# Performance work log

Measured on AMD Instinct MI355X. Metric: run time of the kernel, lower is better.

## Reference

```python
import jax, jax.numpy as jnp
import numpy as np
from jax import lax

STRIDE = 1
PADDING = 1


def setup_inputs() -> dict:
    key = jax.random.key(0)
    k1, k2 = jax.random.split(key)
    x = jax.random.normal(k1, (32, 128, 56, 56), dtype=jnp.float32)
    weight = jax.random.normal(k2, (256, 128, 3, 3), dtype=jnp.float32)
    bias = jnp.zeros((256,), dtype=jnp.float32)
    return {"x": x, "weight": weight, "bias": bias}


def reference(x, weight, bias):
    # Standard 2D cross-correlation (the intended math of the torch
    # unfold + broadcast-multiply + sum implementation):
    #   out[b,o,h,w] = sum_{i,kh,kw} x_pad[b,i,h*s+kh,w*s+kw] * weight[o,i,kh,kw] + bias[o]
    out = lax.conv_general_dilated(
        x, weight,
        window_strides=(STRIDE, STRIDE),
        padding=[(PADDING, PADDING), (PADDING, PADDING)],
        dimension_numbers=("NCHW", "OIHW", "NCHW"),
    )
    return out + bias[None, :, None, None]
```

## Files before the change

### kernel.cpp

```cpp
#include <hip/hip_runtime.h>
#include <cstdint>
#include <cstddef>

#define NB    32
#define CI    128
#define CO    256
#define HW_   56
#define HP    58
#define KTOT  1152
#define NKT   36
#define MTOT  (NB * HW_ * HW_)

static constexpr size_t XP_ELEMS = (size_t)NB * HP * HP * CI;
static constexpr size_t WT_ELEMS = (size_t)CO * KTOT;
static constexpr size_t XP_BYTES = XP_ELEMS * 2;
static constexpr size_t WT_BYTES = WT_ELEMS * 2;

typedef __attribute__((ext_vector_type(8))) short bf16x8;
typedef __attribute__((ext_vector_type(4))) float f32x4;

__device__ __forceinline__ short f32_to_bf16(float f) {
  uint32_t u = __float_as_uint(f);
  uint32_t r = (u + 0x7FFFu + ((u >> 16) & 1u)) >> 16;
  return (short)r;
}

typedef __attribute__((address_space(3))) void       lds_void;
typedef const __attribute__((address_space(1))) void gbl_void;

__device__ __forceinline__ void gload16(const void* g, void* l) {
  __builtin_amdgcn_global_load_lds((gbl_void*)g, (lds_void*)l, 16, 0, 0);
}

__global__ void pad_convert(const float* __restrict__ x, short* __restrict__ xp) {
  __shared__ float lds[CI][57];
  const int blk = blockIdx.x;
  const int hp  = blk % HP;
  const int nb  = blk / HP;
  const int tid = threadIdx.x;
  const bool interior = (hp >= 1 && hp <= HW_);
  if (interior) {
    const float* src = x + (size_t)nb * CI * HW_ * HW_ + (size_t)(hp - 1) * HW_;
    for (int t = tid; t < CI * HW_; t += 256) {
      int c = t / HW_, w = t % HW_;
      lds[c][w] = src[(size_t)c * HW_ * HW_ + w];
    }
  }
  __syncthreads();
  short* dst = xp + (size_t)(nb * HP + hp) * HP * CI;
  for (int t = tid; t < HP * CI; t += 256) {
    int wp = t >> 7, c = t & 127;
    float v = 0.f;
    if (interior && wp >= 1 && wp <= HW_) v = lds[c][wp - 1];
    dst[t] = f32_to_bf16(v);
  }
}

__global__ void wt_convert(const float* __restrict__ wt, short* __restrict__ wbT) {
  int idx = blockIdx.x * 256 + threadIdx.x;
  int c  = idx & 127;
  int t  = idx >> 7;
  int kw = t % 3;  int t2 = t / 3;
  int kh = t2 % 3; int o  = t2 / 3;
  wbT[idx] = f32_to_bf16(wt[(((size_t)o * CI + c) * 3 + kh) * 3 + kw]);
}

__device__ __forceinline__ int tap_off_bytes(int u) {
  const int tap = u >> 2;
  const int cq  = u & 3;
  const int kh  = tap / 3, kw = tap - kh * 3;
  return ((kh * HP + kw) * CI + cq * 32) * 2;
}

__global__ __launch_bounds__(256, 2) void conv_gemm(
    const short* __restrict__ xp, const short* __restrict__ wbT,
    const float* __restrict__ bias, float* __restrict__ out) {
  __shared__ __align__(16) char lds[3 * 24576];

  const int tid = threadIdx.x;
  const int l   = tid & 63;
  const int wv  = tid >> 6;
  const int wm  = wv >> 1, wn = wv & 1;
  const int mt  = blockIdx.x;

  const int piece = l & 3;
  const int srow  = wv * 16 + (l >> 2);
  const char* aP0; const char* aP1;
  {
    int r0 = srow, r1 = 64 + srow;
    int m0 = mt * 128 + r0, m1 = mt * 128 + r1;
    int nb0 = m0 / 3136, hw0 = m0 - nb0 * 3136, h0 = hw0 / HW_, w0 = hw0 - (hw0 / HW_) * HW_;
    int nb1 = m1 / 3136, hw1 = m1 - nb1 * 3136, h1 = hw1 / HW_, w1 = hw1 - (hw1 / HW_) * HW_;
    aP0 = (const char*)xp + ((size_t)((nb0 * HP + h0) * HP + w0) * CI + piece * 8) * 2;
    aP1 = (const char*)xp + ((size_t)((nb1 * HP + h1) * HP + w1) * CI + piece * 8) * 2;
  }
  const char* bP0 = (const char*)wbT + ((size_t)(  0 + srow) * KTOT + piece * 8) * 2;
  const char* bP1 = (const char*)wbT + ((size_t)( 64 + srow) * KTOT + piece * 8) * 2;
  const char* bP2 = (const char*)wbT + ((size_t)(128 + srow) * KTOT + piece * 8) * 2;
  const char* bP3 = (const char*)wbT + ((size_t)(192 + srow) * KTOT + piece * 8) * 2;

  const int raOff = (wm * 64  + (l & 15)) * 64 + (l >> 4) * 16;
  const int rbOff = (wn * 128 + (l & 15)) * 64 + (l >> 4) * 16;

  char* B0 = lds;
  char* B1 = lds + 24576;
  char* B2 = lds + 49152;

#define STAGE(U, BUF)                                                        \
  {                                                                          \
    const int aoff_ = tap_off_bytes(U);                                      \
    const int boff_ = (U) * 64;                                              \
    char* sA_ = (BUF) + wv * 1024;                                           \
    gload16(aP0 + aoff_, sA_);                                               \
    gload16(aP1 + aoff_, sA_ + 4096);                                        \
    char* sB_ = (BUF) + 8192 + wv * 1024;                                    \
    gload16(bP0 + boff_, sB_);                                               \
    gload16(bP1 + boff_, sB_ + 4096);                                        \
    gload16(bP2 + boff_, sB_ + 8192);                                        \
    gload16(bP3 + boff_, sB_ + 12288);                                       \
  }

  f32x4 acc[4][8];
#pragma unroll
  for (int g = 0; g < 4; ++g)
#pragma unroll
    for (int h = 0; h < 8; ++h) acc[g][h] = {0.f, 0.f, 0.f, 0.f};

  STAGE(0, B0)
  STAGE(1, B1)
  asm volatile("s_waitcnt vmcnt(6)" ::: "memory");
  __builtin_amdgcn_s_barrier();
  __builtin_amdgcn_sched_barrier(0);

#define TILE_BODY(V, CUR, STG)                                               \
  {                                                                          \
    const int v_ = (V);                                                      \
    if (v_ + 2 < NKT) STAGE(v_ + 2, STG)                                     \
    bf16x8 af[4], bf[8];                                                     \
    _Pragma("unroll") for (int g = 0; g < 4; ++g)                            \
        af[g] = *(const bf16x8*)((CUR) + raOff + g * 1024);                  \
    _Pragma("unroll") for (int h = 0; h < 8; ++h)                            \
        bf[h] = *(const bf16x8*)((CUR) + 8192 + rbOff + h * 1024);           \
    __builtin_amdgcn_s_setprio(1);                                           \
    _Pragma("unroll") for (int g = 0; g < 4; ++g)                            \
      _Pragma("unroll") for (int h = 0; h < 8; ++h)                          \
        acc[g][h] = __builtin_amdgcn_mfma_f32_16x16x32_bf16(                 \
            bf[h], af[g], acc[g][h], 0, 0, 0);                               \
    __builtin_amdgcn_s_setprio(0);                                           \
    if (v_ < NKT - 1) {                                                      \
      if (v_ == NKT - 2) { asm volatile("s_waitcnt vmcnt(0)" ::: "memory"); }\
      else               { asm volatile("s_waitcnt vmcnt(6)" ::: "memory"); }\
      __builtin_amdgcn_s_barrier();                                          \
      __builtin_amdgcn_sched_barrier(0);                                     \
    }                                                                        \
  }

  for (int v3 = 0; v3 < NKT; v3 += 3) {
    TILE_BODY(v3 + 0, B0, B2)
    TILE_BODY(v3 + 1, B1, B0)
    TILE_BODY(v3 + 2, B2, B1)
  }

  const int mBase = mt * 128 + wm * 64 + (l & 15);
  const int ocB   = wn * 128 + (l >> 4) * 4;
#pragma unroll
  for (int g = 0; g < 4; ++g) {
    const int m  = mBase + g * 16;
    const int nb = m / 3136;
    const int hw = m - nb * 3136;
    float* op = out + (size_t)nb * CO * 3136 + hw;
#pragma unroll
    for (int h = 0; h < 8; ++h) {
      const int oc = ocB + h * 16;
#pragma unroll
      for (int j = 0; j < 4; ++j)
        op[(size_t)(oc + j) * 3136] = acc[g][h][j] + bias[oc + j];
    }
  }
#undef TILE_BODY
#undef STAGE
}

__global__ void conv_naive(const float* __restrict__ x, const float* __restrict__ wt,
                           const float* __restrict__ bias, float* __restrict__ out) {
  const int idx = blockIdx.x * 256 + threadIdx.x;
  if (idx >= NB * CO * 3136) return;
  const int w  = idx % HW_;
  const int h  = (idx / HW_) % HW_;
  const int oc = (idx / 3136) % CO;
  const int nb = idx / (3136 * CO);
  float s = bias[oc];
  for (int c = 0; c < CI; ++c)
    for (int kh = 0; kh < 3; ++kh) {
      const int ih = h + kh - 1;
      if (ih < 0 || ih >= HW_) continue;
      for (int kw = 0; kw < 3; ++kw) {
        const int iw = w + kw - 1;
        if (iw < 0 || iw >= HW_) continue;
        s += x[((size_t)(nb * CI + c) * HW_ + ih) * HW_ + iw] *
             wt[(((size_t)oc * CI + c) * 3 + kh) * 3 + kw];
      }
    }
  out[idx] = s;
}

extern "C" void kernel_launch(void* const* d_in, const int* in_sizes, int n_in,
                              void* d_out, int out_size, void* d_ws, size_t ws_size,
                              hipStream_t stream) {
  const float* x    = (const float*)d_in[0];
  const float* wt   = (const float*)d_in[1];
  const float* bias = (const float*)d_in[2];
  float* out        = (float*)d_out;

  if (ws_size < XP_BYTES + WT_BYTES) {
    conv_naive<<<(NB * CO * 3136 + 255) / 256, 256, 0, stream>>>(x, wt, bias, out);
    return;
  }

  short* xp  = (short*)d_ws;
  short* wbT = (short*)((char*)d_ws + XP_BYTES);

  pad_convert<<<NB * HP, 256, 0, stream>>>(x, xp);
  wt_convert<<<(int)(WT_ELEMS / 256), 256, 0, stream>>>(wt, wbT);
  conv_gemm<<<MTOT / 128, 256, 0, stream>>>(xp, wbT, bias, out);
}
```

Measured before the change: 103.4 us.

## Enlarge conv GEMM tile to 256x256 with 8 waves, 4-stage LDS pipeline and swizzle

The implicit-GEMM kernel moves from 128x256 tiles with 4 waves to 256x256 tiles with 8 waves. It uses a 4-deep LDS ring with XOR-swizzled layout, and register double-buffering that splits each k-step into two MFMA halves overlapped with loads. Blocks are remapped so that neighbouring block IDs are spread across the M dimension, and the bias values are hoisted into registers. The aim is better operand reuse, fewer LDS bank conflicts and better latency hiding. In exchange it uses 128KB of LDS per block, so likely only one block fits per CU, and it adds more barriers.

Result: faster. 97.02 us (-6.2%).

```diff
diff --git a/kernel.cpp b/kernel.cpp
--- a/kernel.cpp
+++ b/kernel.cpp
@@ -65,120 +65,141 @@
   wbT[idx] = f32_to_bf16(wt[(((size_t)o * CI + c) * 3 + kh) * 3 + kw]);
 }
 
-__device__ __forceinline__ int tap_off_bytes(int u) {
+__device__ __forceinline__ int stage_aoff(int u) {
   const int tap = u >> 2;
   const int cq  = u & 3;
   const int kh  = tap / 3, kw = tap - kh * 3;
   return ((kh * HP + kw) * CI + cq * 32) * 2;
 }
 
-__global__ __launch_bounds__(256, 2) void conv_gemm(
+__global__ __launch_bounds__(512, 2) void conv_gemm(
     const short* __restrict__ xp, const short* __restrict__ wbT,
     const float* __restrict__ bias, float* __restrict__ out) {
-  __shared__ __align__(16) char lds[3 * 24576];
+  __shared__ __align__(16) char lds_[4 * 32768];
 
   const int tid = threadIdx.x;
   const int l   = tid & 63;
   const int wv  = tid >> 6;
-  const int wm  = wv >> 1, wn = wv & 1;
-  const int mt  = blockIdx.x;
-
-  const int piece = l & 3;
-  const int srow  = wv * 16 + (l >> 2);
-  const char* aP0; const char* aP1;
+  const int wm  = wv >> 2;
+  const int wn  = wv & 3;
+
+  const int bid = blockIdx.x;
+  const int mt  = (bid & 7) * 49 + (bid >> 3);
+
+  const int pcs = (((tid & 3) ^ ((tid >> 3) & 3)) << 4);
+  const char *aSrc0, *aSrc1;
   {
-    int r0 = srow, r1 = 64 + srow;
-    int m0 = mt * 128 + r0, m1 = mt * 128 + r1;
+    int r0 = tid >> 2, r1 = 128 + (tid >> 2);
+    int m0 = mt * 256 + r0, m1 = mt * 256 + r1;
     int nb0 = m0 / 3136, hw0 = m0 - nb0 * 3136, h0 = hw0 / HW_, w0 = hw0 - (hw0 / HW_) * HW_;
     int nb1 = m1 / 3136, hw1 = m1 - nb1 * 3136, h1 = hw1 / HW_, w1 = hw1 - (hw1 / HW_) * HW_;
-    aP0 = (const char*)xp + ((size_t)((nb0 * HP + h0) * HP + w0) * CI + piece * 8) * 2;
-    aP1 = (const char*)xp + ((size_t)((nb1 * HP + h1) * HP + w1) * CI + piece * 8) * 2;
-  }
-  const char* bP0 = (const char*)wbT + ((size_t)(  0 + srow) * KTOT + piece * 8) * 2;
-  const char* bP1 = (const char*)wbT + ((size_t)( 64 + srow) * KTOT + piece * 8) * 2;
-  const char* bP2 = (const char*)wbT + ((size_t)(128 + srow) * KTOT + piece * 8) * 2;
-  const char* bP3 = (const char*)wbT + ((size_t)(192 + srow) * KTOT + piece * 8) * 2;
-
-  const int raOff = (wm * 64  + (l & 15)) * 64 + (l >> 4) * 16;
-  const int rbOff = (wn * 128 + (l & 15)) * 64 + (l >> 4) * 16;
-
-  char* B0 = lds;
-  char* B1 = lds + 24576;
-  char* B2 = lds + 49152;
-
-#define STAGE(U, BUF)                                                        \
+    aSrc0 = (const char*)xp + ((size_t)((nb0 * HP + h0) * HP + w0) * CI) * 2 + pcs;
+    aSrc1 = (const char*)xp + ((size_t)((nb1 * HP + h1) * HP + w1) * CI) * 2 + pcs;
+  }
+  const char* bSrc0 = (const char*)wbT + (size_t)(tid >> 2) * KTOT * 2 + pcs;
+  const char* bSrc1 = (const char*)wbT + (size_t)(128 + (tid >> 2)) * KTOT * 2 + pcs;
+
+  const int lm   = l & 15;
+  const int koff = (((l >> 4) ^ ((l >> 1) & 3)) << 4);
+  const int raOff = (wm * 128 + lm) * 64 + koff;
+  const int rbOff = (wn * 64 + lm) * 64 + koff;
+
+#define STAGE_HALF(U, G)                                                     \
   {                                                                          \
-    const int aoff_ = tap_off_bytes(U);                                      \
-    const int boff_ = (U) * 64;                                              \
-    char* sA_ = (BUF) + wv * 1024;                                           \
-    gload16(aP0 + aoff_, sA_);                                               \
-    gload16(aP1 + aoff_, sA_ + 4096);                                        \
-    char* sB_ = (BUF) + 8192 + wv * 1024;                                    \
-    gload16(bP0 + boff_, sB_);                                               \
-    gload16(bP1 + boff_, sB_ + 4096);                                        \
-    gload16(bP2 + boff_, sB_ + 8192);                                        \
-    gload16(bP3 + boff_, sB_ + 12288);                                       \
-  }
-
-  f32x4 acc[4][8];
-#pragma unroll
-  for (int g = 0; g < 4; ++g)
-#pragma unroll
-    for (int h = 0; h < 8; ++h) acc[g][h] = {0.f, 0.f, 0.f, 0.f};
-
-  STAGE(0, B0)
-  STAGE(1, B1)
-  asm volatile("s_waitcnt vmcnt(6)" ::: "memory");
+    char* dA_ = lds_ + ((U) & 3) * 32768 + (G) * 8192 + wv * 1024;           \
+    gload16(aSrc##G + stage_aoff(U), dA_);                                   \
+    gload16(bSrc##G + (size_t)(U) * 64, dA_ + 16384);                        \
+  }
+
+  f32x4 acc[8][4];
+#pragma unroll
+  for (int g = 0; g < 8; ++g)
+#pragma unroll
+    for (int h = 0; h < 4; ++h) acc[g][h] = {0.f, 0.f, 0.f, 0.f};
+
+  STAGE_HALF(0, 0) STAGE_HALF(0, 1)
+  STAGE_HALF(1, 0) STAGE_HALF(1, 1)
+  STAGE_HALF(2, 0) STAGE_HALF(2, 1)
+  asm volatile("s_waitcnt vmcnt(4)" ::: "memory");
   __builtin_amdgcn_s_barrier();
   __builtin_amdgcn_sched_barrier(0);
 
-#define TILE_BODY(V, CUR, STG)                                               \
+  bf16x8 afA[4], afB[4], bfP[4], bfQ[4];
+  {
+    const char* bA_ = lds_;
+#pragma unroll
+    for (int g = 0; g < 4; ++g) afA[g] = *(const bf16x8*)(bA_ + raOff + g * 1024);
+#pragma unroll
+    for (int h = 0; h < 4; ++h) bfP[h] = *(const bf16x8*)(bA_ + 16384 + rbOff + h * 1024);
+  }
+
+#define TILE_(V, BFC, BFN)                                                   \
   {                                                                          \
     const int v_ = (V);                                                      \
-    if (v_ + 2 < NKT) STAGE(v_ + 2, STG)                                     \
-    bf16x8 af[4], bf[8];                                                     \
-    _Pragma("unroll") for (int g = 0; g < 4; ++g)                            \
-        af[g] = *(const bf16x8*)((CUR) + raOff + g * 1024);                  \
-    _Pragma("unroll") for (int h = 0; h < 8; ++h)                            \
-        bf[h] = *(const bf16x8*)((CUR) + 8192 + rbOff + h * 1024);           \
+                 \
+    if (v_ + 3 < NKT) STAGE_HALF(v_ + 3, 0)                                  \
+    { const char* bA_ = lds_ + (v_ & 3) * 32768;                             \
+      _Pragma("unroll") for (int g = 0; g < 4; ++g)                          \
+        afB[g] = *(const bf16x8*)(bA_ + raOff + 4096 + g * 1024); }          \
+    __builtin_amdgcn_s_barrier();                                            \
+    __builtin_amdgcn_sched_barrier(0);                                       \
     __builtin_amdgcn_s_setprio(1);                                           \
     _Pragma("unroll") for (int g = 0; g < 4; ++g)                            \
-      _Pragma("unroll") for (int h = 0; h < 8; ++h)                          \
+      _Pragma("unroll") for (int h = 0; h < 4; ++h)                          \
         acc[g][h] = __builtin_amdgcn_mfma_f32_16x16x32_bf16(                 \
-            bf[h], af[g], acc[g][h], 0, 0, 0);                               \
+            BFC[h], afA[g], acc[g][h], 0, 0, 0);                             \
     __builtin_amdgcn_s_setprio(0);                                           \
-    if (v_ < NKT - 1) {                                                      \
-      if (v_ == NKT - 2) { asm volatile("s_waitcnt vmcnt(0)" ::: "memory"); }\
-      else               { asm volatile("s_waitcnt vmcnt(6)" ::: "memory"); }\
-      __builtin_amdgcn_s_barrier();                                          \
-      __builtin_amdgcn_sched_barrier(0);                                     \
+    __builtin_amdgcn_sched_barrier(0);                                       \
+                 \
+    if (v_ + 3 < NKT) STAGE_HALF(v_ + 3, 1)                                  \
+    if (v_ + 1 < NKT) {                                                      \
+      const char* bA_ = lds_ + ((v_ + 1) & 3) * 32768;                       \
+      _Pragma("unroll") for (int g = 0; g < 4; ++g)                          \
+        afA[g] = *(const bf16x8*)(bA_ + raOff + g * 1024);                   \
+      _Pragma("unroll") for (int h = 0; h < 4; ++h)                          \
+        BFN[h] = *(const bf16x8*)(bA_ + 16384 + rbOff + h * 1024);           \
     }                                                                        \
-  }
-
-  for (int v3 = 0; v3 < NKT; v3 += 3) {
-    TILE_BODY(v3 + 0, B0, B2)
-    TILE_BODY(v3 + 1, B1, B0)
-    TILE_BODY(v3 + 2, B2, B1)
-  }
-
-  const int mBase = mt * 128 + wm * 64 + (l & 15);
-  const int ocB   = wn * 128 + (l >> 4) * 4;
-#pragma unroll
-  for (int g = 0; g < 4; ++g) {
+    if (v_ <= NKT - 4)      { asm volatile("s_waitcnt vmcnt(4)" ::: "memory"); } \
+    else if (v_ == NKT - 3) { asm volatile("s_waitcnt vmcnt(0)" ::: "memory"); } \
+    __builtin_amdgcn_s_barrier();                                            \
+    __builtin_amdgcn_sched_barrier(0);                                       \
+    __builtin_amdgcn_s_setprio(1);                                           \
+    _Pragma("unroll") for (int g = 0; g < 4; ++g)                            \
+      _Pragma("unroll") for (int h = 0; h < 4; ++h)                          \
+        acc[4 + g][h] = __builtin_amdgcn_mfma_f32_16x16x32_bf16(             \
+            BFC[h], afB[g], acc[4 + g][h], 0, 0, 0);                         \
+    __builtin_amdgcn_s_setprio(0);                                           \
+    __builtin_amdgcn_sched_barrier(0);                                       \
+  }
+
+  for (int t = 0; t < NKT / 2; ++t) {
+    TILE_(2 * t,     bfP, bfQ)
+    TILE_(2 * t + 1, bfQ, bfP)
+  }
+#undef TILE_
+#undef STAGE_HALF
+
+  const int mBase = mt * 256 + wm * 128 + lm;
+  const int ocB   = wn * 64 + (l >> 4) * 4;
+  float bv[4][4];
+#pragma unroll
+  for (int h = 0; h < 4; ++h)
+#pragma unroll
+    for (int j = 0; j < 4; ++j) bv[h][j] = bias[ocB + h * 16 + j];
+#pragma unroll
+  for (int g = 0; g < 8; ++g) {
     const int m  = mBase + g * 16;
     const int nb = m / 3136;
     const int hw = m - nb * 3136;
     float* op = out + (size_t)nb * CO * 3136 + hw;
 #pragma unroll
-    for (int h = 0; h < 8; ++h) {
+    for (int h = 0; h < 4; ++h) {
       const int oc = ocB + h * 16;
 #pragma unroll
       for (int j = 0; j < 4; ++j)
-        op[(size_t)(oc + j) * 3136] = acc[g][h][j] + bias[oc + j];
+        op[(size_t)(oc + j) * 3136] = acc[g][h][j] + bv[h][j];
     }
   }
-#undef TILE_BODY
-#undef STAGE
 }
 
 __global__ void conv_naive(const float* __restrict__ x, const float* __restrict__ wt,
@@ -222,5 +243,5 @@
 
   pad_convert<<<NB * HP, 256, 0, stream>>>(x, xp);
   wt_convert<<<(int)(WT_ELEMS / 256), 256, 0, stream>>>(wt, wbT);
-  conv_gemm<<<MTOT / 128, 256, 0, stream>>>(xp, wbT, bias, out);
-}
+  conv_gemm<<<MTOT / 256, 512, 0, stream>>>(xp, wbT, bias, out);
+}
```
